# Optimization experiments

Hardware: AMD Instinct MI355X
Metric: run time of the kernel (lower is better)

The kernel has to match this reference:

```python
import jax, jax.numpy as jnp
import numpy as np

EMBED_DIM = 768


def setup_inputs() -> dict:
    key = jax.random.key(0)
    k1, k2, k3, k4, k5 = jax.random.split(key, 5)
    C = EMBED_DIM
    B, N = 32, 1024
    s = 1.0 / np.sqrt(C)
    x = jax.random.normal(k1, (B, N, C), dtype=jnp.float32)
    qkv_w = jax.random.normal(k2, (C, 3 * C), dtype=jnp.float32) * s  # [in, out]
    qkv_b = jax.random.normal(k3, (3 * C,), dtype=jnp.float32) * 0.02
    proj_w = jax.random.normal(k4, (C, C), dtype=jnp.float32) * s
    proj_b = jax.random.normal(k5, (C,), dtype=jnp.float32) * 0.02
    return {"x": x, "qkv_w": qkv_w, "qkv_b": qkv_b, "proj_w": proj_w, "proj_b": proj_b}


def reference(x, qkv_w, qkv_b, proj_w, proj_b):
    B, N, C = x.shape
    qkv = (x @ qkv_w + qkv_b).reshape(B, N, 3, C)
    q, k, v = qkv[:, :, 0], qkv[:, :, 1], qkv[:, :, 2]  # each [B, N, C]
    # single-head full attention; scale by sqrt(C) as in source
    scores = jnp.einsum('bnc,bmc->bnm', q, k) / jnp.sqrt(jnp.asarray(C, x.dtype))
    attn = jax.nn.softmax(scores, axis=-1)  # dropout p=0.0 -> identity
    out = jnp.einsum('bnm,bmc->bnc', attn, v)
    # faithful to source: transpose(1,2).reshape(B,N,C) permutes the data
    out = jnp.swapaxes(out, 1, 2).reshape(B, N, C)
    return out @ proj_w + proj_b
```

## Files before the change

### kernel.cpp

```cpp
#include <hip/hip_runtime.h>
#include <hip/hip_bf16.h>


#define BM 256
#define BN 256
#define BKK 64

typedef __attribute__((ext_vector_type(8))) short bf16x8;
typedef __attribute__((ext_vector_type(4))) float f32x4;

__device__ __forceinline__ unsigned short f2b(float f) {
  unsigned int u = __float_as_uint(f);
  u = u + 0x7fffu + ((u >> 16) & 1u);
  return (unsigned short)(u >> 16);
}

__device__ __forceinline__ void g2l16(const void* g, void* l) {
  __builtin_amdgcn_global_load_lds(
      (const __attribute__((address_space(1))) unsigned int*)g,
      (__attribute__((address_space(3))) unsigned int*)l, 16, 0, 0);
}

template <int EPI>
__global__ __launch_bounds__(512, 2) void gemm_nt8(
    const unsigned short* __restrict__ A, const unsigned short* __restrict__ B,
    unsigned short* __restrict__ Cb, unsigned short* __restrict__ Ck,
    unsigned short* __restrict__ Cv, float* __restrict__ Cf,
    const float* __restrict__ bias, float* __restrict__ Z, int K, int lda,
    int ldb, int ldc, long bsA, long bsB, long bsC, float scale, int MT,
    int NN) {
  __shared__ unsigned short As[2][BM][BKK];
  __shared__ unsigned short Bs[2][BN][BKK];

  const int id = blockIdx.x;
  const int w = (id & 7) * ((int)gridDim.x >> 3) + (id >> 3);
  const int pb = MT * NN;
  const int bz = w / pb;
  const int r = w - bz * pb;
  const int bym = r / NN;
  const int bxn = r - bym * NN;

  const unsigned short* Ag = A + (long)bz * bsA + (long)(bym * BM) * lda;
  const unsigned short* Bg = B + (long)bz * bsB + (long)(bxn * BN) * ldb;

  const int tid = threadIdx.x;
  const int wave = tid >> 6;
  const int lane = tid & 63;
  const int l15 = lane & 15;
  const int lk = lane >> 4;
  const int wm = (wave >> 2) << 7;
  const int wn = (wave & 3) << 6;

  const int sr = lane >> 3;
  const int sc = (lane & 7) ^ sr;

  f32x4 acc[8][4];
#pragma unroll
  for (int m = 0; m < 8; ++m)
#pragma unroll
    for (int n = 0; n < 4; ++n)
#pragma unroll
      for (int p = 0; p < 4; ++p) acc[m][n][p] = 0.f;

  auto stA = [&](int d, int h, int k0) {
#pragma unroll
    for (int i = 0; i < 2; ++i) {
      const int rb = (h << 7) + (wave << 4) + (i << 3);
      g2l16(Ag + (long)(rb + sr) * lda + k0 + (sc << 3), &As[d][rb][0]);
    }
  };
  auto stB = [&](int d, int h, int k0) {
#pragma unroll
    for (int i = 0; i < 2; ++i) {
      const int rb = (h << 7) + (wave << 4) + (i << 3);
      g2l16(Bg + (long)(rb + sr) * ldb + k0 + (sc << 3), &Bs[d][rb][0]);
    }
  };
  auto ldA = [&](int d, int m, int ks) {
    return *(const bf16x8*)&As[d][wm + (m << 4) + l15]
                              [((((ks << 2) | lk) ^ (l15 & 7)) << 3)];
  };
  auto ldB = [&](int d, int n, int ks) {
    return *(const bf16x8*)&Bs[d][wn + (n << 4) + l15]
                              [((((ks << 2) | lk) ^ (l15 & 7)) << 3)];
  };

  const int NT = K / BKK;
  stA(0, 0, 0); stA(0, 1, 0); stB(0, 0, 0); stB(0, 1, 0);
  stA(1, 0, BKK); stA(1, 1, BKK); stB(1, 0, BKK); stB(1, 1, BKK);
  asm volatile("s_waitcnt vmcnt(8)" ::: "memory");
  __builtin_amdgcn_sched_barrier(0);
  __builtin_amdgcn_s_barrier();
  __builtin_amdgcn_sched_barrier(0);

  int cur = 0;
  for (int t = 0; t < NT; ++t) {
    const bool st2 = (t + 2 < NT);
    const int k2 = (t + 2) * BKK;

    bf16x8 bv[4][2], aL[4][2];
#pragma unroll
    for (int n = 0; n < 4; ++n)
#pragma unroll
      for (int ks = 0; ks < 2; ++ks) bv[n][ks] = ldB(cur, n, ks);
#pragma unroll
    for (int m = 0; m < 4; ++m)
#pragma unroll
      for (int ks = 0; ks < 2; ++ks) aL[m][ks] = ldA(cur, m, ks);

    __builtin_amdgcn_s_setprio(1);
#pragma unroll
    for (int m = 0; m < 4; ++m)
#pragma unroll
      for (int n = 0; n < 4; ++n)
#pragma unroll
        for (int ks = 0; ks < 2; ++ks)
          acc[m][n] = __builtin_amdgcn_mfma_f32_16x16x32_bf16(
              aL[m][ks], bv[n][ks], acc[m][n], 0, 0, 0);
    __builtin_amdgcn_s_setprio(0);

    bf16x8 aH[4][2];
#pragma unroll
    for (int m = 0; m < 4; ++m)
#pragma unroll
      for (int ks = 0; ks < 2; ++ks) aH[m][ks] = ldA(cur, m + 4, ks);

    __builtin_amdgcn_s_setprio(1);
#pragma unroll
    for (int m = 0; m < 4; ++m)
#pragma unroll
      for (int n = 0; n < 4; ++n)
#pragma unroll
        for (int ks = 0; ks < 2; ++ks)
          acc[m + 4][n] = __builtin_amdgcn_mfma_f32_16x16x32_bf16(
              aH[m][ks], bv[n][ks], acc[m + 4][n], 0, 0, 0);
    __builtin_amdgcn_s_setprio(0);

    __builtin_amdgcn_s_barrier();
    __builtin_amdgcn_sched_barrier(0);
    if (st2) {
      stB(cur, 0, k2); stB(cur, 1, k2);
      stA(cur, 0, k2); stA(cur, 1, k2);
    }
    if (st2)
      asm volatile("s_waitcnt vmcnt(8)" ::: "memory");
    else
      asm volatile("s_waitcnt vmcnt(0)" ::: "memory");
    __builtin_amdgcn_sched_barrier(0);
    __builtin_amdgcn_s_barrier();
    __builtin_amdgcn_sched_barrier(0);
    cur ^= 1;
  }

  const int row0 = bym * BM + wm + (lk << 2);
  const int col0 = bxn * BN + wn;

  if constexpr (EPI == 1) {
    const int seg = (bxn * BN) / 768;
    unsigned short* O = (seg == 0) ? Cb : ((seg == 1) ? Ck : Cv);
    float bv2[4];
#pragma unroll
    for (int n = 0; n < 4; ++n) bv2[n] = bias[col0 + (n << 4) + l15];
    const int cl0 = col0 + l15 - seg * 768;
#pragma unroll
    for (int m = 0; m < 8; ++m)
#pragma unroll
      for (int p = 0; p < 4; ++p) {
        const long rr = row0 + (m << 4) + p;
#pragma unroll
        for (int n = 0; n < 4; ++n)
          O[rr * 768 + cl0 + (n << 4)] = f2b(acc[m][n][p] + bv2[n]);
      }
  } else if constexpr (EPI == 2) {
    float bv2[4];
#pragma unroll
    for (int n = 0; n < 4; ++n) bv2[n] = bias[col0 + (n << 4) + l15];
#pragma unroll
    for (int m = 0; m < 8; ++m)
#pragma unroll
      for (int p = 0; p < 4; ++p) {
        const long rr = row0 + (m << 4) + p;
#pragma unroll
        for (int n = 0; n < 4; ++n)
          Cf[rr * ldc + col0 + (n << 4) + l15] = acc[m][n][p] + bv2[n];
      }
  } else if constexpr (EPI == 3) {
    unsigned short* C = Cb + (long)bz * bsC;
#pragma unroll
    for (int m = 0; m < 8; ++m) {
      float es[4] = {0.f, 0.f, 0.f, 0.f};
#pragma unroll
      for (int p = 0; p < 4; ++p) {
        const long rr = row0 + (m << 4) + p;
#pragma unroll
        for (int n = 0; n < 4; ++n) {
          const float e = __expf(acc[m][n][p] * scale);
          es[p] += e;
          C[rr * ldc + col0 + (n << 4) + l15] = f2b(e);
        }
      }
#pragma unroll
      for (int p = 0; p < 4; ++p) {
        float s = es[p];
        s += __shfl_xor(s, 1);
        s += __shfl_xor(s, 2);
        s += __shfl_xor(s, 4);
        s += __shfl_xor(s, 8);
        if (l15 == 0)
          atomicAdd(&Z[(long)bz * 1024 + row0 + (m << 4) + p], s);
      }
    }
  } else {
    unsigned short* C = Cb + (long)bz * bsC;
    float zv[4];
#pragma unroll
    for (int n = 0; n < 4; ++n)
      zv[n] = 1.f / Z[(long)bz * 1024 + col0 + (n << 4) + l15];
#pragma unroll
    for (int m = 0; m < 8; ++m)
#pragma unroll
      for (int p = 0; p < 4; ++p) {
        const long rr = row0 + (m << 4) + p;
#pragma unroll
        for (int n = 0; n < 4; ++n)
          C[rr * ldc + col0 + (n << 4) + l15] = f2b(acc[m][n][p] * zv[n]);
      }
  }
}

__global__ __launch_bounds__(256) void prep(
    const float4* __restrict__ x, ushort4* __restrict__ x_bf,
    const float* __restrict__ qkv_w, unsigned short* __restrict__ Wqkv,
    const float* __restrict__ proj_w, unsigned short* __restrict__ Wp) {
  const int blk = blockIdx.x;
  if (blk < 24576) {
    const long i = (long)blk * 256 + threadIdx.x;
    float4 f = x[i];
    ushort4 o;
    o.x = f2b(f.x); o.y = f2b(f.y); o.z = f2b(f.z); o.w = f2b(f.w);
    x_bf[i] = o;
  } else if (blk < 24576 + 6912) {
    const long i = (long)(blk - 24576) * 256 + threadIdx.x;
    const int k = (int)(i % 768);
    const int j = (int)(i / 768);
    Wqkv[i] = f2b(qkv_w[(long)k * 2304 + j]);
  } else {
    const long i = (long)(blk - 24576 - 6912) * 256 + threadIdx.x;
    const int k = (int)(i % 768);
    const int j = (int)(i / 768);
    Wp[i] = f2b(proj_w[(long)k * 768 + j]);
  }
}

__global__ __launch_bounds__(256) void transpose_v(
    const unsigned short* __restrict__ V, unsigned short* __restrict__ Vt) {
  __shared__ unsigned short T[64][72];
  const int b = blockIdx.z;
  const int d0 = blockIdx.x << 6;
  const int m0 = blockIdx.y << 6;
  const unsigned short* Vb = V + (long)b * 786432;
  unsigned short* Vtb = Vt + (long)b * 786432;
  const int tid = threadIdx.x;
  const int r = tid >> 2;
  const int c4 = tid & 3;
#pragma unroll
  for (int h = 0; h < 2; ++h) {
    const int cc = (c4 + (h << 2)) << 3;
    *(uint4*)&T[r][cc] = *(const uint4*)&Vb[(long)(m0 + r) * 768 + d0 + cc];
  }
  __syncthreads();
#pragma unroll
  for (int h = 0; h < 2; ++h) {
    const int mm = (c4 + (h << 2)) << 3;
    alignas(16) unsigned short tmp[8];
#pragma unroll
    for (int e = 0; e < 8; ++e) tmp[e] = T[mm + e][r];
    *(uint4*)&Vtb[(long)(d0 + r) * 1024 + m0 + mm] = *(uint4*)tmp;
  }
}

extern "C" void kernel_launch(void* const* d_in, const int* in_sizes, int n_in,
                              void* d_out, int out_size, void* d_ws,
                              size_t ws_size, hipStream_t stream) {
  const float* x = (const float*)d_in[0];
  const float* qkv_w = (const float*)d_in[1];
  const float* qkv_b = (const float*)d_in[2];
  const float* proj_w = (const float*)d_in[3];
  const float* proj_b = (const float*)d_in[4];
  float* out = (float*)d_out;

  char* ws = (char*)d_ws;
  unsigned short* x_bf = (unsigned short*)ws;
  unsigned short* Wqkv = (unsigned short*)(ws + 50331648);
  unsigned short* Wp = (unsigned short*)(ws + 53870592);
  unsigned short* Qb = (unsigned short*)(ws + 55050240);
  unsigned short* Kb = (unsigned short*)(ws + 105381888);
  unsigned short* Vb = (unsigned short*)(ws + 155713536);
  unsigned short* Sb = (unsigned short*)(ws + 206045184);
  unsigned short* Vt = x_bf;
  unsigned short* Hb = Qb;
  float* Zs = (float*)Vb;

  prep<<<33792, 256, 0, stream>>>((const float4*)x, (ushort4*)x_bf, qkv_w,
                                  Wqkv, proj_w, Wp);

  gemm_nt8<1><<<1152, 512, 0, stream>>>(
      x_bf, Wqkv, Qb, Kb, Vb, nullptr, qkv_b, nullptr, 768, 768, 768, 0, 0, 0,
      0, 1.f, 128, 9);

  transpose_v<<<dim3(12, 16, 32), 256, 0, stream>>>(Vb, Vt);

  hipMemsetAsync(Zs, 0, 32 * 1024 * sizeof(float), stream);

  gemm_nt8<3><<<512, 512, 0, stream>>>(
      Qb, Kb, Sb, nullptr, nullptr, nullptr, nullptr, Zs, 768, 768, 768, 1024,
      786432, 786432, 1048576, 0.03608439182435161f, 4, 4);

  gemm_nt8<4><<<384, 512, 0, stream>>>(
      Vt, Sb, Hb, nullptr, nullptr, nullptr, nullptr, Zs, 1024, 1024, 1024,
      1024, 786432, 1048576, 786432, 1.f, 3, 4);

  gemm_nt8<2><<<384, 512, 0, stream>>>(
      Hb, Wp, nullptr, nullptr, nullptr, out, proj_b, nullptr, 768, 768, 768,
      768, 0, 0, 0, 1.f, 128, 3);
}
```

Measured before the change: 559.3 us.

## Split GEMM inner loop into quadrants and prefetch next tile's fragments early

Splits each k-tile's 8x4 MFMA block into four quadrants, ordered so LDS fragment loads overlap with MFMA work. The next tile's low A/B fragments are loaded right after the barrier and before the last quadrant's MFMAs, so LDS latency is hidden across the tile boundary. The cost is more live registers (fragments kept across iterations) plus extra sched_barriers, which could cut occupancy at 2 blocks per CU or cause spills.

```diff
diff --git a/kernel.cpp b/kernel.cpp
--- a/kernel.cpp
+++ b/kernel.cpp
@@ -93,47 +93,64 @@
   __builtin_amdgcn_s_barrier();
   __builtin_amdgcn_sched_barrier(0);
 
+  bf16x8 aLo[4][2], bLo[2][2];
+#pragma unroll
+  for (int m = 0; m < 4; ++m)
+#pragma unroll
+    for (int ks = 0; ks < 2; ++ks) aLo[m][ks] = ldA(0, m, ks);
+#pragma unroll
+  for (int n = 0; n < 2; ++n)
+#pragma unroll
+    for (int ks = 0; ks < 2; ++ks) bLo[n][ks] = ldB(0, n, ks);
+
   int cur = 0;
   for (int t = 0; t < NT; ++t) {
+    const int nxt = cur ^ 1;
     const bool st2 = (t + 2 < NT);
     const int k2 = (t + 2) * BKK;
 
-    bf16x8 bv[4][2], aL[4][2];
-#pragma unroll
-    for (int n = 0; n < 4; ++n)
-#pragma unroll
-      for (int ks = 0; ks < 2; ++ks) bv[n][ks] = ldB(cur, n, ks);
-#pragma unroll
-    for (int m = 0; m < 4; ++m)
-#pragma unroll
-      for (int ks = 0; ks < 2; ++ks) aL[m][ks] = ldA(cur, m, ks);
+    bf16x8 bHi[2][2];
+#pragma unroll
+    for (int n = 0; n < 2; ++n)
+#pragma unroll
+      for (int ks = 0; ks < 2; ++ks) bHi[n][ks] = ldB(cur, n + 2, ks);
+    __builtin_amdgcn_sched_barrier(0);
 
     __builtin_amdgcn_s_setprio(1);
 #pragma unroll
     for (int m = 0; m < 4; ++m)
 #pragma unroll
-      for (int n = 0; n < 4; ++n)
+      for (int n = 0; n < 2; ++n)
 #pragma unroll
         for (int ks = 0; ks < 2; ++ks)
           acc[m][n] = __builtin_amdgcn_mfma_f32_16x16x32_bf16(
-              aL[m][ks], bv[n][ks], acc[m][n], 0, 0, 0);
+              aLo[m][ks], bLo[n][ks], acc[m][n], 0, 0, 0);
     __builtin_amdgcn_s_setprio(0);
 
-    bf16x8 aH[4][2];
-#pragma unroll
-    for (int m = 0; m < 4; ++m)
-#pragma unroll
-      for (int ks = 0; ks < 2; ++ks) aH[m][ks] = ldA(cur, m + 4, ks);
+    bf16x8 aHi[4][2];
+#pragma unroll
+    for (int m = 0; m < 4; ++m)
+#pragma unroll
+      for (int ks = 0; ks < 2; ++ks) aHi[m][ks] = ldA(cur, m + 4, ks);
+    __builtin_amdgcn_sched_barrier(0);
 
     __builtin_amdgcn_s_setprio(1);
 #pragma unroll
     for (int m = 0; m < 4; ++m)
 #pragma unroll
-      for (int n = 0; n < 4; ++n)
+      for (int n = 0; n < 2; ++n)
+#pragma unroll
+        for (int ks = 0; ks < 2; ++ks)
+          acc[m][n + 2] = __builtin_amdgcn_mfma_f32_16x16x32_bf16(
+              aLo[m][ks], bHi[n][ks], acc[m][n + 2], 0, 0, 0);
+#pragma unroll
+    for (int m = 0; m < 4; ++m)
+#pragma unroll
+      for (int n = 0; n < 2; ++n)
 #pragma unroll
         for (int ks = 0; ks < 2; ++ks)
           acc[m + 4][n] = __builtin_amdgcn_mfma_f32_16x16x32_bf16(
-              aH[m][ks], bv[n][ks], acc[m + 4][n], 0, 0, 0);
+              aHi[m][ks], bLo[n][ks], acc[m + 4][n], 0, 0, 0);
     __builtin_amdgcn_s_setprio(0);
 
     __builtin_amdgcn_s_barrier();
@@ -149,7 +166,30 @@
     __builtin_amdgcn_sched_barrier(0);
     __builtin_amdgcn_s_barrier();
     __builtin_amdgcn_sched_barrier(0);
-    cur ^= 1;
+
+    if (t + 1 < NT) {
+#pragma unroll
+      for (int m = 0; m < 4; ++m)
+#pragma unroll
+        for (int ks = 0; ks < 2; ++ks) aLo[m][ks] = ldA(nxt, m, ks);
+#pragma unroll
+      for (int n = 0; n < 2; ++n)
+#pragma unroll
+        for (int ks = 0; ks < 2; ++ks) bLo[n][ks] = ldB(nxt, n, ks);
+      __builtin_amdgcn_sched_barrier(0);
+    }
+
+    __builtin_amdgcn_s_setprio(1);
+#pragma unroll
+    for (int m = 0; m < 4; ++m)
+#pragma unroll
+      for (int n = 0; n < 2; ++n)
+#pragma unroll
+        for (int ks = 0; ks < 2; ++ks)
+          acc[m + 4][n + 2] = __builtin_amdgcn_mfma_f32_16x16x32_bf16(
+              aHi[m][ks], bHi[n][ks], acc[m + 4][n + 2], 0, 0, 0);
+    __builtin_amdgcn_s_setprio(0);
+    cur = nxt;
   }
 
   const int row0 = bym * BM + wm + (lk << 2);
```

After: 562.8 us. Within noise of the previous version (+0.6%).
